# Performance work log

Measured on AMD Instinct MI355X. Metric: run time of the kernel, lower is better.

## Reference

```python
import jax, jax.numpy as jnp
import numpy as np
import math

B, S, H, NH, DH, FF = 8, 512, 1024, 16, 64, 4096


def _layer_norm(x, gamma, beta, eps=1e-12):
    m = jnp.mean(x, axis=-1, keepdims=True)
    v = jnp.mean(jnp.square(x - m), axis=-1, keepdims=True)
    return (x - m) * jax.lax.rsqrt(v + eps) * gamma + beta


def setup_inputs() -> dict:
    key = jax.random.key(0)
    ks = jax.random.split(key, 12)
    w = lambda k, shape: jax.random.normal(k, shape, jnp.float32) * 0.02
    return {
        "layer_input": jax.random.normal(ks[0], (B * S, H), jnp.float32),
        "attention_mask": jax.random.randint(ks[1], (B, S, S), 0, 2, jnp.int32),
        "Wq": w(ks[2], (H, H)), "bq": jnp.zeros((H,), jnp.float32),
        "Wk": w(ks[3], (H, H)), "bk": jnp.zeros((H,), jnp.float32),
        "Wv": w(ks[4], (H, H)), "bv": jnp.zeros((H,), jnp.float32),
        "Wao": w(ks[5], (H, H)), "bao": jnp.zeros((H,), jnp.float32),
        "gamma1": jnp.ones((H,), jnp.float32), "beta1": jnp.zeros((H,), jnp.float32),
        "Wi": w(ks[6], (H, FF)), "bi": jnp.zeros((FF,), jnp.float32),
        "Wo": w(ks[7], (FF, H)), "bo": jnp.zeros((H,), jnp.float32),
        "gamma2": jnp.ones((H,), jnp.float32), "beta2": jnp.zeros((H,), jnp.float32),
        "batch_size": B,
        "seq_length": S,
    }


def reference(layer_input, attention_mask, Wq, bq, Wk, bk, Wv, bv, Wao, bao,
              gamma1, beta1, Wi, bi, Wo, bo, gamma2, beta2, batch_size, seq_length):
    Bs, Sl = batch_size, seq_length
    # QKV projections on flattened [B*S, H]
    q = layer_input @ Wq + bq
    k = layer_input @ Wk + bk
    v = layer_input @ Wv + bv
    # [B*S, H] -> [B, NH, S, DH]
    split = lambda t: t.reshape(Bs, Sl, NH, DH).transpose(0, 2, 1, 3)
    qh, kh, vh = split(q), split(k), split(v)
    # scaled dot-product scores [B, NH, S, S]
    scores = jnp.einsum("bhqd,bhkd->bhqk", qh, kh) * (1.0 / math.sqrt(DH))
    adder = (1.0 - attention_mask[:, None].astype(jnp.float32)) * -10000.0
    probs = jax.nn.softmax(scores + adder, axis=-1)
    # context [B, NH, S, DH] -> [B*S, H]
    ctx = jnp.einsum("bhqk,bhkd->bhqd", probs, vh)
    ctx = ctx.transpose(0, 2, 1, 3).reshape(Bs * Sl, NH * DH)
    attn_out = _layer_norm(ctx @ Wao + bao + layer_input, gamma1, beta1)
    inter = jax.nn.gelu(attn_out @ Wi + bi, approximate=True)  # BERT tanh-gelu
    out = _layer_norm(inter @ Wo + bo + attn_out, gamma2, beta2)
    return out
```

## Files before the change

kernel.cpp:

```cpp
#include <hip/hip_runtime.h>
#include <stdint.h>
#include <math.h>

typedef __attribute__((ext_vector_type(8))) short bf16x8;
typedef __attribute__((ext_vector_type(4))) float f32x4;
typedef __attribute__((ext_vector_type(4))) unsigned short us4;
typedef __attribute__((ext_vector_type(8))) unsigned short us8;

#define BB   8
#define SS   512
#define HH   1024
#define NHH  16
#define DHH  64
#define FFF  4096
#define MTOK 4096
#define QKVN 3072

__device__ __forceinline__ unsigned short f2bf(float f) {
  union { float f; uint32_t u; } c; c.f = f;
  uint32_t u = c.u;
  return (unsigned short)((u + 0x7fffu + ((u >> 16) & 1u)) >> 16);
}
__device__ __forceinline__ float bf2f(unsigned short u) {
  union { uint32_t u; float f; } c; c.u = ((uint32_t)u) << 16; return c.f;
}

__device__ __forceinline__ float gelu_tanh(float x) {
  float u = 0.7978845608028654f * (x + 0.044715f * x * x * x);
  return x / (1.0f + __expf(-2.0f * u));
}

__device__ __forceinline__ void gload16(const unsigned short* g, unsigned short* l) {
  __builtin_amdgcn_global_load_lds(
      (const __attribute__((address_space(1))) unsigned short*)g,
      (__attribute__((address_space(3))) unsigned short*)l, 16, 0, 0);
}

__global__ void cast_f32_to_bf16(const float* __restrict__ in,
                                 unsigned short* __restrict__ out, int n4) {
  int i = blockIdx.x * blockDim.x + threadIdx.x;
  if (i >= n4) return;
  f32x4 v = *(const f32x4*)(in + (size_t)i * 4);
  us4 o;
  #pragma unroll
  for (int j = 0; j < 4; ++j) o[j] = f2bf(v[j]);
  *(us4*)(out + (size_t)i * 4) = o;
}

__global__ void mask_to_adder(const int* __restrict__ mask,
                              unsigned short* __restrict__ out, int n8) {
  int i = blockIdx.x * 256 + threadIdx.x;
  if (i >= n8) return;
  us8 o;
  #pragma unroll
  for (int j = 0; j < 8; ++j)
    o[j] = f2bf((float)(1 - mask[(size_t)i * 8 + j]) * -10000.0f - 8.0f);
  *(us8*)(out + (size_t)i * 8) = o;
}

__global__ void prep_weights(
    const float* __restrict__ Wq, const float* __restrict__ Wk,
    const float* __restrict__ Wv, const float* __restrict__ Wao,
    const float* __restrict__ Wi, const float* __restrict__ Wo,
    const float* __restrict__ bq, const float* __restrict__ bk,
    const float* __restrict__ bv,
    unsigned short* __restrict__ WqkvT, unsigned short* __restrict__ WaoT,
    unsigned short* __restrict__ WiT, unsigned short* __restrict__ WoT,
    float* __restrict__ bqkv) {
  __shared__ float tile[32][33];
  const int bid = blockIdx.x;
  const int tx = threadIdx.x, ty = threadIdx.y;
  if (bid >= 12288) {
    int i = (bid - 12288) * 256 + ty * 32 + tx;
    bqkv[i] = i < HH ? bq[i] : (i < 2 * HH ? bk[i - HH] : bv[i - 2 * HH]);
    return;
  }
  const float* src; unsigned short* dst; int R, C, bx, by;
  if (bid < 4096) {
    int w6 = bid >> 10, i = bid & 1023;
    src = w6 == 0 ? Wq : w6 == 1 ? Wk : w6 == 2 ? Wv : Wao;
    dst = w6 == 3 ? WaoT : WqkvT + (size_t)w6 * HH * HH;
    R = HH; C = HH; bx = i & 31; by = i >> 5;
  } else if (bid < 8192) {
    int i = bid - 4096; src = Wi; dst = WiT; R = HH; C = FFF; bx = i & 127; by = i >> 7;
  } else {
    int i = bid - 8192; src = Wo; dst = WoT; R = FFF; C = HH; bx = i & 31; by = i >> 5;
  }
  const int bc = bx * 32, br = by * 32;
  #pragma unroll
  for (int i = 0; i < 32; i += 8)
    tile[ty + i][tx] = src[(size_t)(br + ty + i) * C + bc + tx];
  __syncthreads();
  #pragma unroll
  for (int i = 0; i < 32; i += 8)
    dst[(size_t)(bc + ty + i) * R + br + tx] = f2bf(tile[tx][ty + i]);
}

template <int EPI>
__global__ __launch_bounds__(256, 2) void gemm4(
    const unsigned short* __restrict__ A, const unsigned short* __restrict__ BT,
    const float* __restrict__ bias, unsigned short* __restrict__ Cb,
    float* __restrict__ Cf, int M, int N, int K, int KSL) {
  __shared__ unsigned short Asl[2][128 * 64];
  __shared__ unsigned short Bsl[2][128 * 64];
  const int t = threadIdx.x;
  const int w = t >> 6, lane = t & 63;
  const int g = lane >> 4, fr = lane & 15;
  const int wr = w >> 1, wc = w & 1;
  const int m0 = blockIdx.x * 128, n0 = blockIdx.y * 128;
  const int k0 = blockIdx.z * KSL;
  const int nk = KSL >> 6;

  const int srow = t >> 3;
  const int schunk = (t & 7) ^ (srow & 7);
  const unsigned short* gA = A + (size_t)(m0 + srow) * K + k0 + schunk * 8;
  const unsigned short* gB = BT + (size_t)(n0 + srow) * K + k0 + schunk * 8;

  f32x4 acc[4][4] = {};

  #define STAGE(buf, kt)                                                 \
    _Pragma("unroll")                                                    \
    for (int j = 0; j < 4; ++j) {                                        \
      gload16(gA + (size_t)(kt) * 64 + (size_t)j * 32 * K,               \
              &Asl[buf][j * 2048 + w * 512]);                            \
      gload16(gB + (size_t)(kt) * 64 + (size_t)j * 32 * K,               \
              &Bsl[buf][j * 2048 + w * 512]);                            \
    }

  STAGE(0, 0);
  for (int kt = 0; kt < nk; ++kt) {
    const int cur = kt & 1;
    if (kt + 1 < nk) {
      STAGE(cur ^ 1, kt + 1);
      asm volatile("s_waitcnt vmcnt(8)" ::: "memory");
    } else {
      asm volatile("s_waitcnt vmcnt(0)" ::: "memory");
    }
    __builtin_amdgcn_s_barrier();
    bf16x8 af[4][2], bfr[4][2];
    #pragma unroll
    for (int m = 0; m < 4; ++m)
      #pragma unroll
      for (int kk = 0; kk < 2; ++kk)
        af[m][kk] = *(const bf16x8*)(
            &Asl[cur][(wr * 64 + m * 16 + fr) * 64 + (((kk * 4 + g) ^ (fr & 7)) * 8)]);
    #pragma unroll
    for (int n = 0; n < 4; ++n)
      #pragma unroll
      for (int kk = 0; kk < 2; ++kk)
        bfr[n][kk] = *(const bf16x8*)(
            &Bsl[cur][(wc * 64 + n * 16 + fr) * 64 + (((kk * 4 + g) ^ (fr & 7)) * 8)]);
    __builtin_amdgcn_s_setprio(1);
    #pragma unroll
    for (int kk = 0; kk < 2; ++kk)
      #pragma unroll
      for (int m = 0; m < 4; ++m)
        #pragma unroll
        for (int n = 0; n < 4; ++n)
          acc[m][n] = __builtin_amdgcn_mfma_f32_16x16x32_bf16(
              af[m][kk], bfr[n][kk], acc[m][n], 0, 0, 0);
    __builtin_amdgcn_s_setprio(0);
    __builtin_amdgcn_s_barrier();
  }
  #undef STAGE

  #pragma unroll
  for (int mf = 0; mf < 4; ++mf) {
    const int gr0 = m0 + wr * 64 + mf * 16 + g * 4;
    #pragma unroll
    for (int nf = 0; nf < 4; ++nf) {
      const int gc = n0 + wc * 64 + nf * 16 + fr;
      const float bb = (EPI == 3) ? 0.f : bias[gc];
      #pragma unroll
      for (int r = 0; r < 4; ++r) {
        float v = acc[mf][nf][r] + bb;
        if (EPI == 2) v = gelu_tanh(v);
        if (EPI == 3)
          Cf[(size_t)blockIdx.z * M * N + (size_t)(gr0 + r) * N + gc] = v;
        else
          Cb[(size_t)(gr0 + r) * N + gc] = f2bf(v);
      }
    }
  }
}

__global__ __launch_bounds__(256) void attn_fused(
    const unsigned short* __restrict__ QKV, const unsigned short* __restrict__ adder,
    unsigned short* __restrict__ ctx) {
  __shared__ unsigned short Ks[64][72];
  __shared__ unsigned short Vt[64][72];
  __shared__ unsigned short Al[64][72];
  __shared__ unsigned short Pl[4][16][72];
  const int t = threadIdx.x, w = t >> 6, lane = t & 63;
  const int g = lane >> 4, fr = lane & 15;
  const int bid = blockIdx.x;
  const int b = bid & 7, h = (bid >> 3) & 15, qt = bid >> 7;
  const int colh = h * 64;
  const int qrow0 = b * SS + qt * 64 + w * 16;

  bf16x8 aq[2];
  #pragma unroll
  for (int ks = 0; ks < 2; ++ks) {
    union { us8 u; bf16x8 b; } cv;
    cv.u = *(const us8*)(QKV + (size_t)(qrow0 + fr) * QKVN + colh + ks * 32 + g * 8);
    #pragma unroll
    for (int j = 0; j < 8; ++j) cv.u[j] = f2bf(bf2f(cv.u[j]) * 0.125f);
    aq[ks] = cv.b;
  }

  float lrow[4] = {0.f, 0.f, 0.f, 0.f};
  f32x4 oacc[4] = {};

  us8 kr[2], vr[2], ar[2];
  #define ALOAD(kt)                                                          \
    _Pragma("unroll")                                                        \
    for (int i = 0; i < 2; ++i) {                                            \
      int c = i * 256 + t, row = c >> 3, ko = (c & 7) * 8;                   \
      const size_t gb = (size_t)(b * SS + (kt) * 64 + row) * QKVN + colh + ko; \
      kr[i] = *(const us8*)(QKV + HH + gb);                                  \
      vr[i] = *(const us8*)(QKV + 2 * HH + gb);                              \
      ar[i] = *(const us8*)(adder + (size_t)(b * SS + qt * 64 + row) * SS + (kt) * 64 + ko); \
    }

  ALOAD(0);
  for (int kt = 0; kt < 8; ++kt) {
    __syncthreads();
    #pragma unroll
    for (int i = 0; i < 2; ++i) {
      int c = i * 256 + t, row = c >> 3, ko = (c & 7) * 8;
      *(us8*)(&Ks[row][ko]) = kr[i];
      *(us8*)(&Al[row][ko]) = ar[i];
      const int xo = (row >> 3) ^ (c & 7);
      #pragma unroll
      for (int j = 0; j < 8; ++j) Vt[ko + j][xo * 8 + (row & 7)] = vr[i][j];
    }
    __syncthreads();
    if (kt < 7) ALOAD(kt + 1);

    f32x4 sacc[4];
    #pragma unroll
    for (int cb = 0; cb < 4; ++cb)
      #pragma unroll
      for (int r = 0; r < 4; ++r)
        sacc[cb][r] = bf2f(Al[w * 16 + g * 4 + r][cb * 16 + fr]);
    #pragma unroll
    for (int ks = 0; ks < 2; ++ks)
      #pragma unroll
      for (int cb = 0; cb < 4; ++cb) {
        bf16x8 bk = *(const bf16x8*)(&Ks[cb * 16 + fr][ks * 32 + g * 8]);
        sacc[cb] = __builtin_amdgcn_mfma_f32_16x16x32_bf16(aq[ks], bk, sacc[cb], 0, 0, 0);
      }

    #pragma unroll
    for (int cb = 0; cb < 4; ++cb)
      #pragma unroll
      for (int r = 0; r < 4; ++r) {
        float pv = __expf(sacc[cb][r]);
        lrow[r] += pv;
        Pl[w][g * 4 + r][cb * 16 + fr] = f2bf(pv);
      }
    asm volatile("s_waitcnt lgkmcnt(0)" ::: "memory");

    #pragma unroll
    for (int ks = 0; ks < 2; ++ks) {
      bf16x8 pa = *(const bf16x8*)(&Pl[w][fr][ks * 32 + g * 8]);
      #pragma unroll
      for (int nb = 0; nb < 4; ++nb) {
        const int dd = nb * 16 + fr;
        const int ch = (ks * 4 + g) ^ ((dd >> 3) & 7);
        bf16x8 bv = *(const bf16x8*)(&Vt[dd][ch * 8]);
        oacc[nb] = __builtin_amdgcn_mfma_f32_16x16x32_bf16(pa, bv, oacc[nb], 0, 0, 0);
      }
    }
  }
  #undef ALOAD

  #pragma unroll
  for (int off = 1; off < 16; off <<= 1)
    #pragma unroll
    for (int r = 0; r < 4; ++r)
      lrow[r] += __shfl_xor(lrow[r], off, 64);

  #pragma unroll
  for (int nb = 0; nb < 4; ++nb)
    #pragma unroll
    for (int r = 0; r < 4; ++r) {
      float v = oacc[nb][r] / lrow[r];
      ctx[(size_t)(qrow0 + g * 4 + r) * HH + colh + nb * 16 + fr] = f2bf(v);
    }
}

__global__ __launch_bounds__(256) void residual_ln_red(
    const float* __restrict__ part, int MN, int S,
    const float* __restrict__ bias, const float* __restrict__ res,
    const float* __restrict__ gamma, const float* __restrict__ beta,
    float* __restrict__ outf, unsigned short* __restrict__ outb) {
  __shared__ float red[8];
  const int row = blockIdx.x, t = threadIdx.x, w = t >> 6, lane = t & 63;
  const size_t base = (size_t)row * HH + t * 4;
  f32x4 v = *(const f32x4*)(res + base);
  v += *(const f32x4*)(bias + t * 4);
  for (int s = 0; s < S; ++s) v += *(const f32x4*)(part + (size_t)s * MN + base);
  float sm = v[0] + v[1] + v[2] + v[3];
  #pragma unroll
  for (int off = 32; off; off >>= 1) sm += __shfl_xor(sm, off, 64);
  if (lane == 0) red[w] = sm;
  __syncthreads();
  const float mean = (red[0] + red[1] + red[2] + red[3]) * (1.0f / HH);
  f32x4 d;
  #pragma unroll
  for (int j = 0; j < 4; ++j) d[j] = v[j] - mean;
  float q = d[0] * d[0] + d[1] * d[1] + d[2] * d[2] + d[3] * d[3];
  #pragma unroll
  for (int off = 32; off; off >>= 1) q += __shfl_xor(q, off, 64);
  if (lane == 0) red[4 + w] = q;
  __syncthreads();
  const float var = (red[4] + red[5] + red[6] + red[7]) * (1.0f / HH);
  const float rstd = rsqrtf(var + 1e-12f);
  f32x4 gv = *(const f32x4*)(gamma + t * 4);
  f32x4 bv = *(const f32x4*)(beta + t * 4);
  f32x4 o;
  #pragma unroll
  for (int j = 0; j < 4; ++j) o[j] = d[j] * rstd * gv[j] + bv[j];
  *(f32x4*)(outf + base) = o;
  if (outb) {
    us4 ob;
    #pragma unroll
    for (int j = 0; j < 4; ++j) ob[j] = f2bf(o[j]);
    *(us4*)(outb + base) = ob;
  }
}

extern "C" void kernel_launch(void* const* d_in, const int* in_sizes, int n_in,
                              void* d_out, int out_size, void* d_ws, size_t ws_size,
                              hipStream_t stream) {
  const float* lin  = (const float*)d_in[0];
  const int* amask  = (const int*)d_in[1];
  const float* Wq   = (const float*)d_in[2];  const float* bq  = (const float*)d_in[3];
  const float* Wk   = (const float*)d_in[4];  const float* bk  = (const float*)d_in[5];
  const float* Wv   = (const float*)d_in[6];  const float* bv  = (const float*)d_in[7];
  const float* Wao  = (const float*)d_in[8];  const float* bao = (const float*)d_in[9];
  const float* g1   = (const float*)d_in[10]; const float* be1 = (const float*)d_in[11];
  const float* Wi   = (const float*)d_in[12]; const float* bi  = (const float*)d_in[13];
  const float* Wo   = (const float*)d_in[14]; const float* bo  = (const float*)d_in[15];
  const float* g2   = (const float*)d_in[16]; const float* be2 = (const float*)d_in[17];

  char* p = (char*)d_ws;
  const size_t MB = 1024ull * 1024;
  unsigned short* Xb    = (unsigned short*)(p + 0);
  unsigned short* WqkvT = (unsigned short*)(p + 8 * MB);
  unsigned short* WaoT  = (unsigned short*)(p + 14 * MB);
  unsigned short* WiT   = (unsigned short*)(p + 16 * MB);
  unsigned short* WoT   = (unsigned short*)(p + 24 * MB);
  unsigned short* QKVb  = (unsigned short*)(p + 32 * MB);
  unsigned short* Ctx   = (unsigned short*)(p + 56 * MB);
  float*          Ao    = (float*)(p + 80 * MB);
  unsigned short* Aob   = (unsigned short*)(p + 96 * MB);
  unsigned short* Inter = (unsigned short*)(p + 104 * MB);
  float*          bqkv  = (float*)(p + 64 * MB);
  unsigned short* adder = (unsigned short*)(p + 66 * MB);
  const int SPL = 2;
  float* PartAO = (float*)(p + 104 * MB);
  float* PartF2 = (float*)(p + 32 * MB);
  (void)in_sizes; (void)n_in; (void)out_size; (void)ws_size;

  cast_f32_to_bf16<<<(MTOK * HH / 4) / 256, 256, 0, stream>>>(lin, Xb, MTOK * HH / 4);
  mask_to_adder<<<(BB * SS * SS / 8) / 256, 256, 0, stream>>>(amask, adder, BB * SS * SS / 8);
  prep_weights<<<12300, dim3(32, 8), 0, stream>>>(Wq, Wk, Wv, Wao, Wi, Wo, bq, bk, bv,
                                                  WqkvT, WaoT, WiT, WoT, bqkv);

  gemm4<0><<<dim3(MTOK / 128, QKVN / 128), 256, 0, stream>>>(
      Xb, WqkvT, bqkv, QKVb, nullptr, MTOK, QKVN, HH, HH);

  attn_fused<<<SS / 64 * BB * NHH, 256, 0, stream>>>(QKVb, adder, Ctx);

  gemm4<3><<<dim3(MTOK / 128, HH / 128, SPL), 256, 0, stream>>>(
      Ctx, WaoT, nullptr, nullptr, PartAO, MTOK, HH, HH, HH / SPL);
  residual_ln_red<<<MTOK, 256, 0, stream>>>(PartAO, MTOK * HH, SPL, bao, lin, g1, be1, Ao, Aob);

  gemm4<2><<<dim3(MTOK / 128, FFF / 128), 256, 0, stream>>>(
      Aob, WiT, bi, Inter, nullptr, MTOK, FFF, HH, HH);

  gemm4<3><<<dim3(MTOK / 128, HH / 128, SPL), 256, 0, stream>>>(
      Inter, WoT, nullptr, nullptr, PartF2, MTOK, HH, FFF, FFF / SPL);
  residual_ln_red<<<MTOK, 256, 0, stream>>>(PartF2, MTOK * HH, SPL, bo, Ao, g2, be2,
                                            (float*)d_out, nullptr);
}
```

Before: 343.1 us.

## Widen GEMM tiles to 128x256 with 8 waves and triple-buffered LDS

Replaces the 128x128, 4-wave GEMM with a 128x256 tile run by 8 waves (512 threads). The new kernel keeps three LDS stages so global loads run two k-steps ahead, with vmcnt waits adjusted to match. The aim is more operand reuse per byte loaded and better hiding of memory latency. In exchange, LDS use rises to about 144KB per block, which limits each CU to one block, and the grids for the QKV, FFN and split-K projections shrink, which may unbalance the waves across CUs.

```diff
diff --git a/kernel.cpp b/kernel.cpp
--- a/kernel.cpp
+++ b/kernel.cpp
@@ -97,17 +97,17 @@
 }
 
 template <int EPI>
-__global__ __launch_bounds__(256, 2) void gemm4(
+__global__ __launch_bounds__(512, 2) void gemm3(
     const unsigned short* __restrict__ A, const unsigned short* __restrict__ BT,
     const float* __restrict__ bias, unsigned short* __restrict__ Cb,
     float* __restrict__ Cf, int M, int N, int K, int KSL) {
-  __shared__ unsigned short Asl[2][128 * 64];
-  __shared__ unsigned short Bsl[2][128 * 64];
+  __shared__ unsigned short Asl[3][128 * 64];
+  __shared__ unsigned short Bsl[3][256 * 64];
   const int t = threadIdx.x;
   const int w = t >> 6, lane = t & 63;
   const int g = lane >> 4, fr = lane & 15;
-  const int wr = w >> 1, wc = w & 1;
-  const int m0 = blockIdx.x * 128, n0 = blockIdx.y * 128;
+  const int wr = w >> 2, wc = w & 3;
+  const int m0 = blockIdx.x * 128, n0 = blockIdx.y * 256;
   const int k0 = blockIdx.z * KSL;
   const int nk = KSL >> 6;
 
@@ -118,21 +118,27 @@
 
   f32x4 acc[4][4] = {};
 
-  #define STAGE(buf, kt)                                                 \
-    _Pragma("unroll")                                                    \
-    for (int j = 0; j < 4; ++j) {                                        \
-      gload16(gA + (size_t)(kt) * 64 + (size_t)j * 32 * K,               \
-              &Asl[buf][j * 2048 + w * 512]);                            \
-      gload16(gB + (size_t)(kt) * 64 + (size_t)j * 32 * K,               \
-              &Bsl[buf][j * 2048 + w * 512]);                            \
-    }
+  #define STAGE(buf, kt)                                                  \
+    do {                                                                  \
+      _Pragma("unroll")                                                   \
+      for (int j = 0; j < 2; ++j)                                         \
+        gload16(gA + (size_t)(kt) * 64 + (size_t)j * 64 * K,              \
+                &Asl[buf][j * 4096 + w * 512]);                           \
+      _Pragma("unroll")                                                   \
+      for (int j = 0; j < 4; ++j)                                         \
+        gload16(gB + (size_t)(kt) * 64 + (size_t)j * 64 * K,              \
+                &Bsl[buf][j * 4096 + w * 512]);                           \
+    } while (0)
 
   STAGE(0, 0);
+  STAGE(1, 1);
+  int cb_ = 0, sb_ = 2;
   for (int kt = 0; kt < nk; ++kt) {
-    const int cur = kt & 1;
-    if (kt + 1 < nk) {
-      STAGE(cur ^ 1, kt + 1);
-      asm volatile("s_waitcnt vmcnt(8)" ::: "memory");
+    if (kt + 2 < nk) {
+      STAGE(sb_, kt + 2);
+      asm volatile("s_waitcnt vmcnt(12)" ::: "memory");
+    } else if (kt + 1 < nk) {
+      asm volatile("s_waitcnt vmcnt(6)" ::: "memory");
     } else {
       asm volatile("s_waitcnt vmcnt(0)" ::: "memory");
     }
@@ -143,13 +149,13 @@
       #pragma unroll
       for (int kk = 0; kk < 2; ++kk)
         af[m][kk] = *(const bf16x8*)(
-            &Asl[cur][(wr * 64 + m * 16 + fr) * 64 + (((kk * 4 + g) ^ (fr & 7)) * 8)]);
+            &Asl[cb_][(wr * 64 + m * 16 + fr) * 64 + (((kk * 4 + g) ^ (fr & 7)) * 8)]);
     #pragma unroll
     for (int n = 0; n < 4; ++n)
       #pragma unroll
       for (int kk = 0; kk < 2; ++kk)
         bfr[n][kk] = *(const bf16x8*)(
-            &Bsl[cur][(wc * 64 + n * 16 + fr) * 64 + (((kk * 4 + g) ^ (fr & 7)) * 8)]);
+            &Bsl[cb_][(wc * 64 + n * 16 + fr) * 64 + (((kk * 4 + g) ^ (fr & 7)) * 8)]);
     __builtin_amdgcn_s_setprio(1);
     #pragma unroll
     for (int kk = 0; kk < 2; ++kk)
@@ -161,6 +167,8 @@
               af[m][kk], bfr[n][kk], acc[m][n], 0, 0, 0);
     __builtin_amdgcn_s_setprio(0);
     __builtin_amdgcn_s_barrier();
+    cb_ = cb_ == 2 ? 0 : cb_ + 1;
+    sb_ = sb_ == 2 ? 0 : sb_ + 1;
   }
   #undef STAGE
 
@@ -369,19 +377,19 @@
   prep_weights<<<12300, dim3(32, 8), 0, stream>>>(Wq, Wk, Wv, Wao, Wi, Wo, bq, bk, bv,
                                                   WqkvT, WaoT, WiT, WoT, bqkv);
 
-  gemm4<0><<<dim3(MTOK / 128, QKVN / 128), 256, 0, stream>>>(
+  gemm3<0><<<dim3(MTOK / 128, QKVN / 256), 512, 0, stream>>>(
       Xb, WqkvT, bqkv, QKVb, nullptr, MTOK, QKVN, HH, HH);
 
   attn_fused<<<SS / 64 * BB * NHH, 256, 0, stream>>>(QKVb, adder, Ctx);
 
-  gemm4<3><<<dim3(MTOK / 128, HH / 128, SPL), 256, 0, stream>>>(
+  gemm3<3><<<dim3(MTOK / 128, HH / 256, SPL), 512, 0, stream>>>(
       Ctx, WaoT, nullptr, nullptr, PartAO, MTOK, HH, HH, HH / SPL);
   residual_ln_red<<<MTOK, 256, 0, stream>>>(PartAO, MTOK * HH, SPL, bao, lin, g1, be1, Ao, Aob);
 
-  gemm4<2><<<dim3(MTOK / 128, FFF / 128), 256, 0, stream>>>(
+  gemm3<2><<<dim3(MTOK / 128, FFF / 256), 512, 0, stream>>>(
       Aob, WiT, bi, Inter, nullptr, MTOK, FFF, HH, HH);
 
-  gemm4<3><<<dim3(MTOK / 128, HH / 128, SPL), 256, 0, stream>>>(
+  gemm3<3><<<dim3(MTOK / 128, HH / 256, SPL), 512, 0, stream>>>(
       Inter, WoT, nullptr, nullptr, PartF2, MTOK, HH, FFF, FFF / SPL);
   residual_ln_red<<<MTOK, 256, 0, stream>>>(PartF2, MTOK * HH, SPL, bo, Ao, g2, be2,
                                             (float*)d_out, nullptr);
```

After: 369.3 us. 1.08x slower.
